# Kernel tuning notes

Measured on AMD Instinct MI355X. Metric: run time of the kernel, lower is better.

## Reference

```python
import jax, jax.numpy as jnp
import numpy as np

# Module constants (from init_kwargs / derived)
KH, KW = 3, 3
STRIDE = (1, 1)
PAD = (1, 1)
DIL = (1, 1)
N_OFFSET_GRPS = 8  # offset.shape[1] // (2*KH*KW) = 144 // 18
N_WEIGHT_GRPS = 1


def setup_inputs() -> dict:
    key = jax.random.key(0)
    k1, k2, k3, k4, k5 = jax.random.split(key, 5)
    B, C, H, W = 4, 64, 128, 128
    inp = {
        "input": jax.random.normal(k1, (B, C, H, W), dtype=jnp.float32),
        "offset": jax.random.normal(k2, (B, 2 * N_OFFSET_GRPS * KH * KW, H, W), dtype=jnp.float32),
        "mask": jax.random.uniform(k3, (B, N_OFFSET_GRPS * KH * KW, H, W), dtype=jnp.float32),
        "weight": jax.random.normal(k4, (64, C, KH, KW), dtype=jnp.float32) * 0.05,
        "bias": jax.random.normal(k5, (64,), dtype=jnp.float32) * 0.05,
    }
    return inp


def _deform_conv2d(x, offset, mask, weight, bias):
    B, C, H, W = x.shape
    Ho, Wo = offset.shape[2], offset.shape[3]
    G = N_OFFSET_GRPS
    K = KH * KW
    Cg = C // G

    # base (un-deformed) sampling positions per kernel tap and output pixel
    ky, kx = jnp.meshgrid(jnp.arange(KH), jnp.arange(KW), indexing="ij")
    ky = ky.reshape(K)
    kx = kx.reshape(K)
    oy = jnp.arange(Ho) * STRIDE[0] - PAD[0]
    ox = jnp.arange(Wo) * STRIDE[1] - PAD[1]
    base_y = (oy[None, :, None] + (ky * DIL[0])[:, None, None]).astype(x.dtype)  # [K,Ho,1]
    base_x = (ox[None, None, :] + (kx * DIL[1])[:, None, None]).astype(x.dtype)  # [K,1,Wo]

    off = offset.reshape(B, G, K, 2, Ho, Wo)  # [...,0]=dy, [...,1]=dx
    py = base_y[None, None] + off[:, :, :, 0]  # [B,G,K,Ho,Wo]
    px = base_x[None, None] + off[:, :, :, 1]

    y0 = jnp.floor(py)
    x0 = jnp.floor(px)
    ly = py - y0  # fractional parts
    lx = px - x0
    y0i = y0.astype(jnp.int32)
    x0i = x0.astype(jnp.int32)

    xg = x.reshape(B, G, Cg, H * W)  # per-offset-group channel slices

    def corner(yi, xi):
        valid = ((yi >= 0) & (yi < H) & (xi >= 0) & (xi < W)).astype(x.dtype)
        idx = jnp.clip(yi, 0, H - 1) * W + jnp.clip(xi, 0, W - 1)  # [B,G,K,Ho,Wo]
        gather = lambda xbg, ibg: xbg[:, ibg]  # [Cg,H*W],[K,Ho,Wo] -> [Cg,K,Ho,Wo]
        v = jax.vmap(jax.vmap(gather))(xg, idx)  # [B,G,Cg,K,Ho,Wo]
        return v * valid[:, :, None]

    w00 = (1 - ly) * (1 - lx)
    w01 = (1 - ly) * lx
    w10 = ly * (1 - lx)
    w11 = ly * lx
    samp = (corner(y0i, x0i) * w00[:, :, None]
            + corner(y0i, x0i + 1) * w01[:, :, None]
            + corner(y0i + 1, x0i) * w10[:, :, None]
            + corner(y0i + 1, x0i + 1) * w11[:, :, None])  # [B,G,Cg,K,Ho,Wo]

    samp = samp * mask.reshape(B, G, 1, K, Ho, Wo)  # DCNv2 modulation
    col = samp.reshape(B, C, K, Ho, Wo)
    wr = weight.reshape(weight.shape[0], C, K)  # groups == 1
    out = jnp.einsum("ock,bckhw->bohw", wr, col) + bias[None, :, None, None]
    return out


def reference(input, offset, mask, weight, bias):
    return _deform_conv2d(input, offset, mask, weight, bias)
```

## Files before the change

kernel.cpp:

```cpp
#include <hip/hip_runtime.h>

#define HH 128
#define WW 128
#define CC 64
#define CO 64
#define BB 4
#define GG 8
#define CG 8
#define KK 9
#define HW (HH*WW)
#define PXT 64

typedef __attribute__((ext_vector_type(8))) short short8;
typedef __attribute__((ext_vector_type(4))) float floatx4;
typedef __attribute__((ext_vector_type(2))) float f32x2;

union S8I { short8 s; int i[4]; };
union FU { float f; unsigned u; };

__device__ inline short f2bf(float f) {
    FU v; v.f = f;
    return (short)((v.u + 0x7FFF + ((v.u >> 16) & 1)) >> 16);
}
__device__ inline unsigned rnd2(float f) {
    FU v; v.f = f;
    return v.u + 0x8000u;
}
__device__ inline float bflo(int e) { union { int i; float f; } u; u.i = e << 16; return u.f; }
__device__ inline float bfhi(int e) { union { int i; float f; } u; u.i = e & 0xffff0000; return u.f; }

__global__ __launch_bounds__(256)
void prep(const float* __restrict__ wt, const float* __restrict__ in,
          short* __restrict__ wf, short* __restrict__ in_t) {
    const int bid = blockIdx.x;
    if (bid < 144) {
        const int tid = bid * 256 + threadIdx.x;
        const int j   = tid & 7;
        const int L   = (tid >> 3) & 63;
        const int fid = tid >> 9;
        const int ot  = fid & 3;
        const int gch = fid >> 2;
        const int h   = gch / 9, gc = gch - h * 9;
        const int o   = ot * 16 + (L & 15);
        const int g   = h * 4 + (L >> 4);
        wf[tid] = f2bf(wt[o * 576 + (g * 8 + j) * 9 + gc]);
    } else {
        const int idx = bid - 144;
        const int bx = idx & 63;
        const int g  = (idx >> 6) & 7;
        const int b  = idx >> 9;
        const int p  = bx * 256 + threadIdx.x;
        const float* src = in + (b * CC + g * CG) * HW + p;
        short8 v;
        #pragma unroll
        for (int cg = 0; cg < CG; ++cg) v[cg] = f2bf(src[cg * HW]);
        *(short8*)(in_t + ((b * GG + g) * HW + p) * 8) = v;
    }
}

__global__ __launch_bounds__(256, 4)
void dcn_fused(const short* __restrict__ in_t, const float* __restrict__ off,
               const float* __restrict__ msk, const short* __restrict__ wf,
               const float* __restrict__ bias, float* __restrict__ out)
{
    const int lin = (blockIdx.x & 7) * 128 + (blockIdx.x >> 3);
    const int b   = lin >> 8;
    const int rem = lin & 255;
    const int ho  = rem >> 1;
    const int bx  = rem & 1;

    const int t  = threadIdx.x;
    const int w = t >> 6, lane = t & 63;
    const int q4 = lane >> 4, n16 = lane & 15;
    const int px = bx * PXT + w * 16 + n16;
    const int basepix = ho * WW + px;

    floatx4 acc[4];
    #pragma unroll
    for (int ot = 0; ot < 4; ++ot)
        #pragma unroll
        for (int r = 0; r < 4; ++r)
            acc[ot][r] = bias[ot * 16 + q4 * 4 + r];

    const char* ib = (const char*)(in_t + (long)b * GG * HW * 8);

    #pragma unroll
    for (int h = 0; h < 2; ++h) {
        const int g = h * 4 + q4;

        float pdy[9], pdx[9], pm[9];
        #pragma unroll
        for (int i = 0; i < 9; ++i) {
            const int offc = (b * 144 + g * 18 + i * 2) * HW + basepix;
            pdy[i] = off[offc];
            pdx[i] = off[offc + HW];
            pm[i]  = msk[(b * 72 + g * 9 + i) * HW + basepix];
        }

        const int gsh = g << 18;
        #pragma unroll
        for (int i = 0; i < 9; ++i) {
            const int ky = i / 3, kx = i - (i / 3) * 3;

            const float py  = (float)(ho - 1 + ky) + pdy[i];
            const float pxf = (float)(px - 1 + kx) + pdx[i];
            const float y0f = floorf(py), x0f = floorf(pxf);
            const float ly = py - y0f, lx = pxf - x0f;
            const int y0 = (int)y0f, x0 = (int)x0f;
            const int y1 = y0 + 1,  x1 = x0 + 1;

            const float vy0 = (y0 >= 0 && y0 < HH) ? 1.f : 0.f;
            const float vy1 = (y1 >= 0 && y1 < HH) ? 1.f : 0.f;
            const float vx0 = (x0 >= 0 && x0 < WW) ? 1.f : 0.f;
            const float vx1 = (x1 >= 0 && x1 < WW) ? 1.f : 0.f;
            const int y0c = min(max(y0, 0), HH - 1), y1c = min(max(y1, 0), HH - 1);
            const int x0c = min(max(x0, 0), WW - 1), x1c = min(max(x1, 0), WW - 1);

            const float m = pm[i];
            const float wy0 = (1.f - ly) * vy0 * m;
            const float wy1 = ly * vy1 * m;
            const float wx0 = (1.f - lx) * vx0;
            const float wx1 = lx * vx1;
            const float w00 = wy0 * wx0, w01 = wy0 * wx1;
            const float w10 = wy1 * wx0, w11 = wy1 * wx1;

            const int y0sh = gsh + (y0c << 11), y1sh = gsh + (y1c << 11);
            const int x0sh = x0c << 4, x1sh = x1c << 4;
            S8I u00, u01, u10, u11;
            u00.s = *(const short8*)(ib + (y0sh + x0sh));
            u01.s = *(const short8*)(ib + (y0sh + x1sh));
            u10.s = *(const short8*)(ib + (y1sh + x0sh));
            u11.s = *(const short8*)(ib + (y1sh + x1sh));

            const f32x2 W00 = {w00, w00}, W01 = {w01, w01};
            const f32x2 W10 = {w10, w10}, W11 = {w11, w11};
            S8I res;
            #pragma unroll
            for (int pc = 0; pc < 4; ++pc) {
                const int e00 = u00.i[pc], e01 = u01.i[pc];
                const int e10 = u10.i[pc], e11 = u11.i[pc];
                f32x2 a00 = {bflo(e00), bfhi(e00)};
                f32x2 a01 = {bflo(e01), bfhi(e01)};
                f32x2 a10 = {bflo(e10), bfhi(e10)};
                f32x2 a11 = {bflo(e11), bfhi(e11)};
                f32x2 v = a00 * W00;
                v += a01 * W01;
                v += a10 * W10;
                v += a11 * W11;
                res.i[pc] = (int)__builtin_amdgcn_perm(rnd2(v.y), rnd2(v.x), 0x07060302u);
            }

            #pragma unroll
            for (int ot = 0; ot < 4; ++ot) {
                const short8 afr = *(const short8*)&wf[((h * 9 + i) * 4 + ot) * 512 + lane * 8];
                acc[ot] = __builtin_amdgcn_mfma_f32_16x16x32_bf16(afr, res.s, acc[ot], 0, 0, 0);
            }
        }
    }

    #pragma unroll
    for (int ot = 0; ot < 4; ++ot)
        #pragma unroll
        for (int r = 0; r < 4; ++r)
            out[((b * CO + ot * 16 + q4 * 4 + r) * HH + ho) * WW + px] = acc[ot][r];
}

extern "C" void kernel_launch(void* const* d_in, const int* in_sizes, int n_in,
                              void* d_out, int out_size, void* d_ws, size_t ws_size,
                              hipStream_t stream) {
    const float* in   = (const float*)d_in[0];
    const float* off  = (const float*)d_in[1];
    const float* msk  = (const float*)d_in[2];
    const float* wt   = (const float*)d_in[3];
    const float* bias = (const float*)d_in[4];
    float* out = (float*)d_out;
    short* wf   = (short*)d_ws;
    short* in_t = (short*)d_ws + 36864;

    prep<<<144 + 2048, 256, 0, stream>>>(wt, in, wf, in_t);

    dcn_fused<<<1024, 256, 0, stream>>>(in_t, off, msk, wf, bias, out);
}
```

Baseline: 146.8 us.

## Batch bilinear gathers across taps and stage weights in LDS

Splits the nine kernel taps into two batches: all 16-byte corner gathers for a batch are issued first, then the blend and MFMA work runs, so more global loads are in flight together. Weight fragments are copied once per block into a 72 KB shared buffer and read from LDS instead of global memory. Launch bounds drop from 4 to 2 blocks per SIMD to allow the larger register footprint. The trade-off is lower occupancy, extra register pressure, and a per-block 72 KB LDS fill before any compute starts.

```diff
diff --git a/kernel.cpp b/kernel.cpp
--- a/kernel.cpp
+++ b/kernel.cpp
@@ -58,18 +58,27 @@
     }
 }
 
-__global__ __launch_bounds__(256, 4)
+__global__ __launch_bounds__(256, 2)
 void dcn_fused(const short* __restrict__ in_t, const float* __restrict__ off,
                const float* __restrict__ msk, const short* __restrict__ wf,
                const float* __restrict__ bias, float* __restrict__ out)
 {
+    __shared__ short s_wf[72 * 512];
+
+    const int t  = threadIdx.x;
+    #pragma unroll
+    for (int k = 0; k < 18; ++k) {
+        const int idx = (k * 256 + t) * 8;
+        *(short8*)(s_wf + idx) = *(const short8*)(wf + idx);
+    }
+    __syncthreads();
+
     const int lin = (blockIdx.x & 7) * 128 + (blockIdx.x >> 3);
     const int b   = lin >> 8;
     const int rem = lin & 255;
     const int ho  = rem >> 1;
     const int bx  = rem & 1;
 
-    const int t  = threadIdx.x;
     const int w = t >> 6, lane = t & 63;
     const int q4 = lane >> 4, n16 = lane & 15;
     const int px = bx * PXT + w * 16 + n16;
@@ -98,62 +107,78 @@
         }
 
         const int gsh = g << 18;
-        #pragma unroll
-        for (int i = 0; i < 9; ++i) {
-            const int ky = i / 3, kx = i - (i / 3) * 3;
-
-            const float py  = (float)(ho - 1 + ky) + pdy[i];
-            const float pxf = (float)(px - 1 + kx) + pdx[i];
-            const float y0f = floorf(py), x0f = floorf(pxf);
-            const float ly = py - y0f, lx = pxf - x0f;
-            const int y0 = (int)y0f, x0 = (int)x0f;
-            const int y1 = y0 + 1,  x1 = x0 + 1;
-
-            const float vy0 = (y0 >= 0 && y0 < HH) ? 1.f : 0.f;
-            const float vy1 = (y1 >= 0 && y1 < HH) ? 1.f : 0.f;
-            const float vx0 = (x0 >= 0 && x0 < WW) ? 1.f : 0.f;
-            const float vx1 = (x1 >= 0 && x1 < WW) ? 1.f : 0.f;
-            const int y0c = min(max(y0, 0), HH - 1), y1c = min(max(y1, 0), HH - 1);
-            const int x0c = min(max(x0, 0), WW - 1), x1c = min(max(x1, 0), WW - 1);
-
-            const float m = pm[i];
-            const float wy0 = (1.f - ly) * vy0 * m;
-            const float wy1 = ly * vy1 * m;
-            const float wx0 = (1.f - lx) * vx0;
-            const float wx1 = lx * vx1;
-            const float w00 = wy0 * wx0, w01 = wy0 * wx1;
-            const float w10 = wy1 * wx0, w11 = wy1 * wx1;
-
-            const int y0sh = gsh + (y0c << 11), y1sh = gsh + (y1c << 11);
-            const int x0sh = x0c << 4, x1sh = x1c << 4;
-            S8I u00, u01, u10, u11;
-            u00.s = *(const short8*)(ib + (y0sh + x0sh));
-            u01.s = *(const short8*)(ib + (y0sh + x1sh));
-            u10.s = *(const short8*)(ib + (y1sh + x0sh));
-            u11.s = *(const short8*)(ib + (y1sh + x1sh));
-
-            const f32x2 W00 = {w00, w00}, W01 = {w01, w01};
-            const f32x2 W10 = {w10, w10}, W11 = {w11, w11};
-            S8I res;
+
+        S8I u00[5], u01[5], u10[5], u11[5];
+        float cw00[5], cw01[5], cw10[5], cw11[5];
+
+        #pragma unroll
+        for (int batch = 0; batch < 2; ++batch) {
+            const int i0 = batch * 5;
+            const int nb = batch ? 4 : 5;
+
             #pragma unroll
-            for (int pc = 0; pc < 4; ++pc) {
-                const int e00 = u00.i[pc], e01 = u01.i[pc];
-                const int e10 = u10.i[pc], e11 = u11.i[pc];
-                f32x2 a00 = {bflo(e00), bfhi(e00)};
-                f32x2 a01 = {bflo(e01), bfhi(e01)};
-                f32x2 a10 = {bflo(e10), bfhi(e10)};
-                f32x2 a11 = {bflo(e11), bfhi(e11)};
-                f32x2 v = a00 * W00;
-                v += a01 * W01;
-                v += a10 * W10;
-                v += a11 * W11;
-                res.i[pc] = (int)__builtin_amdgcn_perm(rnd2(v.y), rnd2(v.x), 0x07060302u);
+            for (int j = 0; j < 5; ++j) {
+                if (j >= nb) break;
+                const int i = i0 + j;
+                const int ky = i / 3, kx = i - (i / 3) * 3;
+
+                const float py  = (float)(ho - 1 + ky) + pdy[i];
+                const float pxf = (float)(px - 1 + kx) + pdx[i];
+                const float y0f = floorf(py), x0f = floorf(pxf);
+                const float ly = py - y0f, lx = pxf - x0f;
+                const int y0 = (int)y0f, x0 = (int)x0f;
+                const int y1 = y0 + 1,  x1 = x0 + 1;
+
+                const float vy0 = (y0 >= 0 && y0 < HH) ? 1.f : 0.f;
+                const float vy1 = (y1 >= 0 && y1 < HH) ? 1.f : 0.f;
+                const float vx0 = (x0 >= 0 && x0 < WW) ? 1.f : 0.f;
+                const float vx1 = (x1 >= 0 && x1 < WW) ? 1.f : 0.f;
+                const int y0c = min(max(y0, 0), HH - 1), y1c = min(max(y1, 0), HH - 1);
+                const int x0c = min(max(x0, 0), WW - 1), x1c = min(max(x1, 0), WW - 1);
+
+                const float m = pm[i];
+                const float wy0 = (1.f - ly) * vy0 * m;
+                const float wy1 = ly * vy1 * m;
+                const float wx0 = (1.f - lx) * vx0;
+                const float wx1 = lx * vx1;
+                cw00[j] = wy0 * wx0; cw01[j] = wy0 * wx1;
+                cw10[j] = wy1 * wx0; cw11[j] = wy1 * wx1;
+
+                const int y0sh = gsh + (y0c << 11), y1sh = gsh + (y1c << 11);
+                const int x0sh = x0c << 4, x1sh = x1c << 4;
+                u00[j].s = *(const short8*)(ib + (y0sh + x0sh));
+                u01[j].s = *(const short8*)(ib + (y0sh + x1sh));
+                u10[j].s = *(const short8*)(ib + (y1sh + x0sh));
+                u11[j].s = *(const short8*)(ib + (y1sh + x1sh));
             }
 
             #pragma unroll
-            for (int ot = 0; ot < 4; ++ot) {
-                const short8 afr = *(const short8*)&wf[((h * 9 + i) * 4 + ot) * 512 + lane * 8];
-                acc[ot] = __builtin_amdgcn_mfma_f32_16x16x32_bf16(afr, res.s, acc[ot], 0, 0, 0);
+            for (int j = 0; j < 5; ++j) {
+                if (j >= nb) break;
+                const int i = i0 + j;
+                const f32x2 W00 = {cw00[j], cw00[j]}, W01 = {cw01[j], cw01[j]};
+                const f32x2 W10 = {cw10[j], cw10[j]}, W11 = {cw11[j], cw11[j]};
+                S8I res;
+                #pragma unroll
+                for (int pc = 0; pc < 4; ++pc) {
+                    const int e00 = u00[j].i[pc], e01 = u01[j].i[pc];
+                    const int e10 = u10[j].i[pc], e11 = u11[j].i[pc];
+                    f32x2 a00 = {bflo(e00), bfhi(e00)};
+                    f32x2 a01 = {bflo(e01), bfhi(e01)};
+                    f32x2 a10 = {bflo(e10), bfhi(e10)};
+                    f32x2 a11 = {bflo(e11), bfhi(e11)};
+                    f32x2 v = a00 * W00;
+                    v += a01 * W01;
+                    v += a10 * W10;
+                    v += a11 * W11;
+                    res.i[pc] = (int)__builtin_amdgcn_perm(rnd2(v.y), rnd2(v.x), 0x07060302u);
+                }
+
+                #pragma unroll
+                for (int ot = 0; ot < 4; ++ot) {
+                    const short8 afr = *(const short8*)&s_wf[((h * 9 + i) * 4 + ot) * 512 + lane * 8];
+                    acc[ot] = __builtin_amdgcn_mfma_f32_16x16x32_bf16(afr, res.s, acc[ot], 0, 0, 0);
+                }
             }
         }
     }
```

Result: faster. 131.1 us (-10.7%).
